# Kernel tuning notes

Measured on AMD Instinct MI355X. Metric: run time of the kernel, lower is better.

Reference implementation:

```python
import jax, jax.numpy as jnp
import numpy as np

N_NODES = 100000
N_EDGES = 3200000
N_FEAT = 512
N_GRAPHS = 64
N_EXTRA_LAYERS = 3  # layers 2..4, all 1->1


def setup_inputs() -> dict:
    key = jax.random.key(0)
    ks = jax.random.split(key, 10)
    x = jax.random.normal(ks[0], (N_NODES, N_FEAT), dtype=jnp.float32)
    edge_src = jax.random.randint(ks[1], (N_EDGES,), 0, N_NODES, dtype=jnp.int32)
    edge_dst = jax.random.randint(ks[2], (N_EDGES,), 0, N_NODES, dtype=jnp.int32)
    graph_ids = jnp.sort(jax.random.randint(ks[3], (N_NODES,), 0, N_GRAPHS, dtype=jnp.int32))
    W_neigh0 = jax.random.normal(ks[4], (N_FEAT, 1), dtype=jnp.float32) * 0.05
    W_self0 = jax.random.normal(ks[5], (N_FEAT, 1), dtype=jnp.float32) * 0.05
    b0 = jax.random.normal(ks[6], (1,), dtype=jnp.float32)
    W_neigh_r = jax.random.normal(ks[7], (N_EXTRA_LAYERS, 1, 1), dtype=jnp.float32)
    W_self_r = jax.random.normal(ks[8], (N_EXTRA_LAYERS, 1, 1), dtype=jnp.float32)
    b_r = jax.random.normal(ks[9], (N_EXTRA_LAYERS, 1), dtype=jnp.float32)
    return {"x": x, "edge_src": edge_src, "edge_dst": edge_dst, "graph_ids": graph_ids,
            "W_neigh0": W_neigh0, "W_self0": W_self0, "b0": b0,
            "W_neigh_r": W_neigh_r, "W_self_r": W_self_r, "b_r": b_r}


def _conv_wl(h, edge_src, edge_dst, W_neigh, W_self, b, n_nodes):
    # GraphConv(norm='none'): project first (in >= out here), gather at src, scatter-sum at dst, + bias
    proj = h @ W_neigh                      # [N, out]
    neigh = jax.ops.segment_sum(proj[edge_src], edge_dst, num_segments=n_nodes) + b
    return neigh + h @ W_self               # residual self-loop linear (no bias)


def reference(x, edge_src, edge_dst, graph_ids, W_neigh0, W_self0, b0, W_neigh_r, W_self_r, b_r):
    n = x.shape[0]
    xs = [x]
    h = jax.nn.relu(_conv_wl(x, edge_src, edge_dst, W_neigh0, W_self0, b0, n))
    xs.append(h)
    for i in range(W_neigh_r.shape[0]):
        h = jax.nn.relu(_conv_wl(h, edge_src, edge_dst, W_neigh_r[i], W_self_r[i], b_r[i], n))
        xs.append(h)
    hcat = jnp.concatenate(xs, axis=1)       # [N, F + num_layers] (concat_features=True)
    # dgl.sum_nodes: per-graph sum over the batched graph
    return jax.ops.segment_sum(hcat, graph_ids, num_segments=N_GRAPHS)  # [G, F + L]
```

## Files before the change

### kernel.cpp

```cpp
#include <hip/hip_runtime.h>

#define N_NODES  100000
#define N_EDGES  3200000
#define N_FEAT   512
#define N_GRAPHS 64
#define N_COLS   516
#define NBINS    1563
#define B1       256
#define EPB      (N_EDGES / B1)
#define CHUNK    25
#define NWAVES   (N_NODES / CHUNK)
#define SRC_MASK 0x1FFFF

__global__ __launch_bounds__(1024) void prep_kernel(
    const int* __restrict__ edst, const int* __restrict__ gid,
    int* __restrict__ histG, int* __restrict__ starts, float* __restrict__ outz)
{
    __shared__ int lh[NBINS];
    const int b = blockIdx.x, tid = threadIdx.x;
    const int gtid = b * 1024 + tid;

    if (gtid < N_GRAPHS * N_COLS) outz[gtid] = 0.f;
    if (gtid < N_NODES) {
        const int g = gid[gtid];
        const int gp = gtid ? gid[gtid - 1] : -1;
        for (int q = gp + 1; q <= g; ++q) starts[q] = gtid;
        if (gtid == N_NODES - 1)
            for (int q = g + 1; q <= N_GRAPHS; ++q) starts[q] = N_NODES;
    }
    for (int i = tid; i < NBINS; i += 1024) lh[i] = 0;
    __syncthreads();
    const int e0 = b * EPB;
    for (int e = e0 + tid; e < e0 + EPB; e += 1024)
        atomicAdd(&lh[edst[e] >> 6], 1);
    __syncthreads();
    for (int i = tid; i < NBINS; i += 1024) histG[i * B1 + b] = lh[i];
}

__device__ __forceinline__ void flush_cs(
    int si, int cur_g, const float a[8], int wave, int lane,
    float* __restrict__ pp, int* __restrict__ pt, float* __restrict__ out)
{
    if (si < 2) {
        const int slot = wave * 2 + si;
        if (lane == 0) pt[slot] = cur_g;
        float* d = pp + (size_t)slot * N_FEAT + lane * 8;
        *(float4*)d       = make_float4(a[0], a[1], a[2], a[3]);
        *(float4*)(d + 4) = make_float4(a[4], a[5], a[6], a[7]);
    } else {
        float* o = out + (size_t)cur_g * N_COLS + lane * 8;
        #pragma unroll
        for (int k = 0; k < 8; ++k) atomicAdd(o + k, a[k]);
    }
}

__global__ __launch_bounds__(256) void pass_x_kernel(
    const float* __restrict__ x, const int* __restrict__ gid,
    const float* __restrict__ wn, const float* __restrict__ ws,
    float* __restrict__ p0, float* __restrict__ s0,
    float* __restrict__ neigh, float* __restrict__ out,
    float* __restrict__ pp, int* __restrict__ pt)
{
    const int wave = (blockIdx.x * blockDim.x + threadIdx.x) >> 6;
    const int lane = threadIdx.x & 63;
    const int start = wave * CHUNK, end = start + CHUNK;

    for (int n = start + lane; n < end; n += 64) neigh[n] = 0.f;

    const float4 wna = *(const float4*)(wn + lane * 8);
    const float4 wnb = *(const float4*)(wn + lane * 8 + 4);
    const float4 wsa = *(const float4*)(ws + lane * 8);
    const float4 wsb = *(const float4*)(ws + lane * 8 + 4);

    float a[8] = {0.f, 0.f, 0.f, 0.f, 0.f, 0.f, 0.f, 0.f};
    int cur_g = gid[start];
    const bool uniform = (gid[end - 1] == cur_g);
    int si = 0;

    for (int n = start; n < end; ++n) {
        if (!uniform) {
            const int g = gid[n];
            if (g != cur_g) {
                flush_cs(si, cur_g, a, wave, lane, pp, pt, out);
                ++si;
                #pragma unroll
                for (int k = 0; k < 8; ++k) a[k] = 0.f;
                cur_g = g;
            }
        }
        const float* row = x + (size_t)n * N_FEAT;
        const float4 xa = *(const float4*)(row + lane * 8);
        const float4 xb = *(const float4*)(row + lane * 8 + 4);

        a[0] += xa.x; a[1] += xa.y; a[2] += xa.z; a[3] += xa.w;
        a[4] += xb.x; a[5] += xb.y; a[6] += xb.z; a[7] += xb.w;

        float dn = xa.x*wna.x + xa.y*wna.y + xa.z*wna.z + xa.w*wna.w
                 + xb.x*wnb.x + xb.y*wnb.y + xb.z*wnb.z + xb.w*wnb.w;
        float dv = xa.x*wsa.x + xa.y*wsa.y + xa.z*wsa.z + xa.w*wsa.w
                 + xb.x*wsb.x + xb.y*wsb.y + xb.z*wsb.z + xb.w*wsb.w;
        #pragma unroll
        for (int off = 32; off > 0; off >>= 1) {
            dn += __shfl_down(dn, off);
            dv += __shfl_down(dv, off);
        }
        if (lane == 0) { p0[n] = dn; s0[n] = dv; }
    }
    flush_cs(si, cur_g, a, wave, lane, pp, pt, out);
    ++si;
    if (lane == 0)
        for (int s2 = si; s2 < 2; ++s2) pt[wave * 2 + s2] = -1;
}

__global__ __launch_bounds__(512) void reduce_x_kernel(
    const float* __restrict__ pp, const int* __restrict__ pt,
    const int* __restrict__ starts, float* __restrict__ out)
{
    const int g = blockIdx.x, c = threadIdx.x;
    const int s = starts[g], e = starts[g + 1];
    float acc = 0.f;
    if (e > s) {
        const int w0 = s / CHUNK, w1 = (e - 1) / CHUNK;
        for (int w = w0; w <= w1; ++w) {
            #pragma unroll
            for (int k = 0; k < 2; ++k) {
                const int slot = w * 2 + k;
                if (pt[slot] == g) acc += pp[(size_t)slot * N_FEAT + c];
            }
        }
    }
    out[(size_t)g * N_COLS + c] += acc;
}

__global__ __launch_bounds__(256) void colscan_kernel(
    const int* __restrict__ histG, int* __restrict__ colscanG,
    int* __restrict__ totalG)
{
    __shared__ int sc[256];
    const int bin = blockIdx.x, t = threadIdx.x;
    const int v = histG[bin * B1 + t];
    sc[t] = v;
    __syncthreads();
    for (int off = 1; off < 256; off <<= 1) {
        const int a = (t >= off) ? sc[t - off] : 0;
        __syncthreads();
        sc[t] += a;
        __syncthreads();
    }
    colscanG[bin * B1 + t] = sc[t] - v;
    if (t == 255) totalG[bin] = sc[255];
}

__global__ __launch_bounds__(256) void scan2_kernel(
    const int* __restrict__ totalG, int* __restrict__ binstart)
{
    __shared__ int sc[256];
    const int t = threadIdx.x;
    const int CH = 7;
    int loc[CH];
    int s = 0;
    for (int i = 0; i < CH; ++i) {
        const int bin = t * CH + i;
        const int v = (bin < NBINS) ? totalG[bin] : 0;
        loc[i] = s; s += v;
    }
    const int my = s;
    sc[t] = my;
    __syncthreads();
    for (int off = 1; off < 256; off <<= 1) {
        const int a = (t >= off) ? sc[t - off] : 0;
        __syncthreads();
        sc[t] += a;
        __syncthreads();
    }
    const int texcl = sc[t] - my;
    for (int i = 0; i < CH; ++i) {
        const int bin = t * CH + i;
        if (bin < NBINS) binstart[bin] = texcl + loc[i];
    }
    if (t == 255) binstart[NBINS] = sc[255];
}

__global__ __launch_bounds__(1024) void reorder_kernel(
    const int* __restrict__ esrc, const int* __restrict__ edst,
    const int* __restrict__ binstart, const int* __restrict__ colscanG,
    int* __restrict__ sorted)
{
    __shared__ int offs[NBINS];
    const int b = blockIdx.x, tid = threadIdx.x;
    for (int i = tid; i < NBINS; i += 1024)
        offs[i] = binstart[i] + colscanG[i * B1 + b];
    __syncthreads();
    const int e0 = b * EPB;
    for (int e = e0 + tid; e < e0 + EPB; e += 1024) {
        const int s = esrc[e], d = edst[e];
        const int p = atomicAdd(&offs[d >> 6], 1);
        sorted[p] = s | ((d & 63) << 17);
    }
}

__global__ __launch_bounds__(256) void binned_scatter_kernel(
    const int* __restrict__ sorted, const int* __restrict__ binstart,
    const float* __restrict__ pin, const float* __restrict__ self_in,
    const float* __restrict__ wself_p, const float* __restrict__ bias_p,
    const float* __restrict__ wnext_p,
    float* __restrict__ h_out, float* __restrict__ p_next,
    const int* __restrict__ gid, float* __restrict__ out, int col)
{
    __shared__ float acc[4][64];
    const int b = blockIdx.x, tid = threadIdx.x;
    ((float*)acc)[tid] = 0.f;
    __syncthreads();

    const int st = binstart[b], en = binstart[b + 1];
    const int w = tid >> 6;
    for (int e = st + tid; e < en; e += 256) {
        const int v = sorted[e];
        atomicAdd(&acc[w][v >> 17], pin[v & SRC_MASK]);
    }
    __syncthreads();

    if (tid < 64) {
        const int n = b * 64 + tid;
        const bool valid = (n < N_NODES);
        float h = 0.f;
        int g = 0;
        if (valid) {
            const float nb = acc[0][tid] + acc[1][tid] + acc[2][tid] + acc[3][tid];
            const float sw = wself_p ? *wself_p : 1.0f;
            const float v = nb + *bias_p + sw * self_in[n];
            h = v > 0.f ? v : 0.f;
            h_out[n] = h;
            if (wnext_p) p_next[n] = h * (*wnext_p);
            g = gid[n];
        }
        const int g0 = __shfl(g, 0);
        if (__all(!valid || g == g0)) {
            float s = h;
            #pragma unroll
            for (int off = 32; off > 0; off >>= 1) s += __shfl_down(s, off);
            if (tid == 0) atomicAdd(&out[(size_t)g0 * N_COLS + col], s);
        } else if (valid) {
            atomicAdd(&out[(size_t)g * N_COLS + col], h);
        }
    }
}

extern "C" void kernel_launch(void* const* d_in, const int* in_sizes, int n_in,
                              void* d_out, int out_size, void* d_ws, size_t ws_size,
                              hipStream_t stream)
{
    (void)in_sizes; (void)n_in; (void)out_size; (void)ws_size;

    const float* x    = (const float*)d_in[0];
    const int*   esrc = (const int*)d_in[1];
    const int*   edst = (const int*)d_in[2];
    const int*   gid  = (const int*)d_in[3];
    const float* Wn0  = (const float*)d_in[4];
    const float* Ws0  = (const float*)d_in[5];
    const float* b0p  = (const float*)d_in[6];
    const float* Wnr  = (const float*)d_in[7];
    const float* Wsr  = (const float*)d_in[8];
    const float* brp  = (const float*)d_in[9];
    float* out = (float*)d_out;

    float* pp    = (float*)d_ws;
    float* bufP  = pp + (size_t)NWAVES * 2 * N_FEAT;
    float* bufP2 = bufP  + N_NODES;
    float* bufS  = bufP2 + N_NODES;
    float* bufH  = bufS  + N_NODES;
    int*   pt       = (int*)(bufH + N_NODES);
    int*   starts   = pt + NWAVES * 2;
    int*   binstart = starts + (N_GRAPHS + 1);
    int*   totalG   = binstart + NBINS + 1;
    int*   histG    = totalG + NBINS;
    int*   colscanG = histG + (size_t)NBINS * B1;
    int*   sorted   = colscanG + (size_t)NBINS * B1;

    prep_kernel<<<B1, 1024, 0, stream>>>(edst, gid, histG, starts, out);
    pass_x_kernel<<<NWAVES / 4, 256, 0, stream>>>(
        x, gid, Wn0, Ws0, bufP, bufS, bufP2 ,
        out, pp, pt);
    colscan_kernel<<<NBINS, 256, 0, stream>>>(histG, colscanG, totalG);
    scan2_kernel<<<1, 256, 0, stream>>>(totalG, binstart);
    reorder_kernel<<<B1, 1024, 0, stream>>>(esrc, edst, binstart, colscanG, sorted);
    reduce_x_kernel<<<N_GRAPHS, 512, 0, stream>>>(pp, pt, starts, out);

    binned_scatter_kernel<<<NBINS, 256, 0, stream>>>(
        sorted, binstart, bufP, bufS, nullptr, b0p, Wnr + 0, bufH, bufP2, gid, out, 512);
    binned_scatter_kernel<<<NBINS, 256, 0, stream>>>(
        sorted, binstart, bufP2, bufH, Wsr + 0, brp + 0, Wnr + 1, bufH, bufP, gid, out, 513);
    binned_scatter_kernel<<<NBINS, 256, 0, stream>>>(
        sorted, binstart, bufP, bufH, Wsr + 1, brp + 1, Wnr + 2, bufH, bufP2, gid, out, 514);
    binned_scatter_kernel<<<NBINS, 256, 0, stream>>>(
        sorted, binstart, bufP2, bufH, Wsr + 2, brp + 2, nullptr, bufH, nullptr, gid, out, 515);
}
```

Baseline: 509.8 us.

## Replace counting-sort edge binning with fixed-capacity buckets fused into feature pass

Drops the histogram, column-scan, global-scan and reorder kernels. Instead, each block writes its edges straight into fixed per-(bin, block) slots of capacity 32, and rare overflows go to a small side list. This bucketing runs in the same launch as the x projection and per-graph column-sum pass. The per-graph reduce of x is folded into the first scatter launch as extra blocks, which cuts the launch count from ten to five. In exchange, each scatter block scans a sparse 8192-slot region plus every block's overflow list. The fixed overflow capacity can silently drop edges if a block overflows more than 64 times.

```diff
diff --git a/kernel.cpp b/kernel.cpp
--- a/kernel.cpp
+++ b/kernel.cpp
@@ -1,4 +1,5 @@
 #include <hip/hip_runtime.h>
+
 
 #define N_NODES  100000
 #define N_EDGES  3200000
@@ -11,228 +12,201 @@
 #define CHUNK    25
 #define NWAVES   (N_NODES / CHUNK)
 #define SRC_MASK 0x1FFFF
-
-__global__ __launch_bounds__(1024) void prep_kernel(
-    const int* __restrict__ edst, const int* __restrict__ gid,
-    int* __restrict__ histG, int* __restrict__ starts, float* __restrict__ outz)
-{
-    __shared__ int lh[NBINS];
-    const int b = blockIdx.x, tid = threadIdx.x;
-    const int gtid = b * 1024 + tid;
-
-    if (gtid < N_GRAPHS * N_COLS) outz[gtid] = 0.f;
-    if (gtid < N_NODES) {
-        const int g = gid[gtid];
-        const int gp = gtid ? gid[gtid - 1] : -1;
-        for (int q = gp + 1; q <= g; ++q) starts[q] = gtid;
-        if (gtid == N_NODES - 1)
-            for (int q = g + 1; q <= N_GRAPHS; ++q) starts[q] = N_NODES;
-    }
-    for (int i = tid; i < NBINS; i += 1024) lh[i] = 0;
-    __syncthreads();
-    const int e0 = b * EPB;
-    for (int e = e0 + tid; e < e0 + EPB; e += 1024)
-        atomicAdd(&lh[edst[e] >> 6], 1);
-    __syncthreads();
-    for (int i = tid; i < NBINS; i += 1024) histG[i * B1 + b] = lh[i];
-}
+#define CAP      32
+#define SLOTS    (B1 * CAP)
+#define OCAP     64
+#define NSLOT    3
 
 __device__ __forceinline__ void flush_cs(
     int si, int cur_g, const float a[8], int wave, int lane,
-    float* __restrict__ pp, int* __restrict__ pt, float* __restrict__ out)
-{
-    if (si < 2) {
-        const int slot = wave * 2 + si;
-        if (lane == 0) pt[slot] = cur_g;
-        float* d = pp + (size_t)slot * N_FEAT + lane * 8;
-        *(float4*)d       = make_float4(a[0], a[1], a[2], a[3]);
-        *(float4*)(d + 4) = make_float4(a[4], a[5], a[6], a[7]);
-    } else {
-        float* o = out + (size_t)cur_g * N_COLS + lane * 8;
-        #pragma unroll
-        for (int k = 0; k < 8; ++k) atomicAdd(o + k, a[k]);
-    }
-}
-
-__global__ __launch_bounds__(256) void pass_x_kernel(
-    const float* __restrict__ x, const int* __restrict__ gid,
+    float* __restrict__ pp, int* __restrict__ pt)
+{
+    const int s = si < NSLOT ? si : NSLOT - 1;
+    const int slot = wave * NSLOT + s;
+    if (lane == 0) pt[slot] = cur_g;
+    float* d = pp + (size_t)slot * N_FEAT + lane * 8;
+    *(float4*)d       = make_float4(a[0], a[1], a[2], a[3]);
+    *(float4*)(d + 4) = make_float4(a[4], a[5], a[6], a[7]);
+}
+
+__global__ __launch_bounds__(256) void fused_k1(
+    const float* __restrict__ x, const int* __restrict__ esrc,
+    const int* __restrict__ edst, const int* __restrict__ gid,
     const float* __restrict__ wn, const float* __restrict__ ws,
     float* __restrict__ p0, float* __restrict__ s0,
-    float* __restrict__ neigh, float* __restrict__ out,
-    float* __restrict__ pp, int* __restrict__ pt)
-{
-    const int wave = (blockIdx.x * blockDim.x + threadIdx.x) >> 6;
-    const int lane = threadIdx.x & 63;
-    const int start = wave * CHUNK, end = start + CHUNK;
-
-    for (int n = start + lane; n < end; n += 64) neigh[n] = 0.f;
-
-    const float4 wna = *(const float4*)(wn + lane * 8);
-    const float4 wnb = *(const float4*)(wn + lane * 8 + 4);
-    const float4 wsa = *(const float4*)(ws + lane * 8);
-    const float4 wsb = *(const float4*)(ws + lane * 8 + 4);
-
-    float a[8] = {0.f, 0.f, 0.f, 0.f, 0.f, 0.f, 0.f, 0.f};
-    int cur_g = gid[start];
-    const bool uniform = (gid[end - 1] == cur_g);
-    int si = 0;
-
-    for (int n = start; n < end; ++n) {
-        if (!uniform) {
-            const int g = gid[n];
-            if (g != cur_g) {
-                flush_cs(si, cur_g, a, wave, lane, pp, pt, out);
-                ++si;
-                #pragma unroll
-                for (int k = 0; k < 8; ++k) a[k] = 0.f;
-                cur_g = g;
-            }
-        }
-        const float* row = x + (size_t)n * N_FEAT;
-        const float4 xa = *(const float4*)(row + lane * 8);
-        const float4 xb = *(const float4*)(row + lane * 8 + 4);
-
-        a[0] += xa.x; a[1] += xa.y; a[2] += xa.z; a[3] += xa.w;
-        a[4] += xb.x; a[5] += xb.y; a[6] += xb.z; a[7] += xb.w;
-
-        float dn = xa.x*wna.x + xa.y*wna.y + xa.z*wna.z + xa.w*wna.w
-                 + xb.x*wnb.x + xb.y*wnb.y + xb.z*wnb.z + xb.w*wnb.w;
-        float dv = xa.x*wsa.x + xa.y*wsa.y + xa.z*wsa.z + xa.w*wsa.w
-                 + xb.x*wsb.x + xb.y*wsb.y + xb.z*wsb.z + xb.w*wsb.w;
-        #pragma unroll
-        for (int off = 32; off > 0; off >>= 1) {
-            dn += __shfl_down(dn, off);
-            dv += __shfl_down(dv, off);
-        }
-        if (lane == 0) { p0[n] = dn; s0[n] = dv; }
-    }
-    flush_cs(si, cur_g, a, wave, lane, pp, pt, out);
-    ++si;
-    if (lane == 0)
-        for (int s2 = si; s2 < 2; ++s2) pt[wave * 2 + s2] = -1;
-}
-
-__global__ __launch_bounds__(512) void reduce_x_kernel(
-    const float* __restrict__ pp, const int* __restrict__ pt,
-    const int* __restrict__ starts, float* __restrict__ out)
-{
-    const int g = blockIdx.x, c = threadIdx.x;
-    const int s = starts[g], e = starts[g + 1];
-    float acc = 0.f;
-    if (e > s) {
-        const int w0 = s / CHUNK, w1 = (e - 1) / CHUNK;
-        for (int w = w0; w <= w1; ++w) {
+    float* __restrict__ out, float* __restrict__ pp, int* __restrict__ pt,
+    int* __restrict__ cntG, int* __restrict__ sorted,
+    int2* __restrict__ ovf, int* __restrict__ ovfcnt,
+    int* __restrict__ starts)
+{
+    __shared__ int cnt[NBINS];
+    __shared__ int ovfc;
+    const int blk = blockIdx.x, tid = threadIdx.x;
+
+    if (blk < 1000) {
+        const int gtid = blk * 256 + tid;
+        if (gtid < N_GRAPHS * N_COLS) out[gtid] = 0.f;
+        if (gtid < N_NODES) {
+            const int g = gid[gtid];
+            const int gp = gtid ? gid[gtid - 1] : -1;
+            for (int q = gp + 1; q <= g; ++q) starts[q] = gtid;
+            if (gtid == N_NODES - 1)
+                for (int q = g + 1; q <= N_GRAPHS; ++q) starts[q] = N_NODES;
+        }
+
+        const int wave = blk * 4 + (tid >> 6);
+        const int lane = tid & 63;
+        const int start = wave * CHUNK, end = start + CHUNK;
+
+        const float4 wna = *(const float4*)(wn + lane * 8);
+        const float4 wnb = *(const float4*)(wn + lane * 8 + 4);
+        const float4 wsa = *(const float4*)(ws + lane * 8);
+        const float4 wsb = *(const float4*)(ws + lane * 8 + 4);
+
+        float a[8] = {0.f, 0.f, 0.f, 0.f, 0.f, 0.f, 0.f, 0.f};
+        int cur_g = gid[start];
+        const bool uniform = (gid[end - 1] == cur_g);
+        int si = 0;
+
+        for (int n = start; n < end; ++n) {
+            if (!uniform) {
+                const int g = gid[n];
+                if (g != cur_g) {
+                    flush_cs(si, cur_g, a, wave, lane, pp, pt);
+                    ++si;
+                    #pragma unroll
+                    for (int k = 0; k < 8; ++k) a[k] = 0.f;
+                    cur_g = g;
+                }
+            }
+            const float* row = x + (size_t)n * N_FEAT;
+            const float4 xa = *(const float4*)(row + lane * 8);
+            const float4 xb = *(const float4*)(row + lane * 8 + 4);
+
+            a[0] += xa.x; a[1] += xa.y; a[2] += xa.z; a[3] += xa.w;
+            a[4] += xb.x; a[5] += xb.y; a[6] += xb.z; a[7] += xb.w;
+
+            float dn = xa.x*wna.x + xa.y*wna.y + xa.z*wna.z + xa.w*wna.w
+                     + xb.x*wnb.x + xb.y*wnb.y + xb.z*wnb.z + xb.w*wnb.w;
+            float dv = xa.x*wsa.x + xa.y*wsa.y + xa.z*wsa.z + xa.w*wsa.w
+                     + xb.x*wsb.x + xb.y*wsb.y + xb.z*wsb.z + xb.w*wsb.w;
             #pragma unroll
-            for (int k = 0; k < 2; ++k) {
-                const int slot = w * 2 + k;
-                if (pt[slot] == g) acc += pp[(size_t)slot * N_FEAT + c];
-            }
-        }
-    }
-    out[(size_t)g * N_COLS + c] += acc;
-}
-
-__global__ __launch_bounds__(256) void colscan_kernel(
-    const int* __restrict__ histG, int* __restrict__ colscanG,
-    int* __restrict__ totalG)
-{
-    __shared__ int sc[256];
-    const int bin = blockIdx.x, t = threadIdx.x;
-    const int v = histG[bin * B1 + t];
-    sc[t] = v;
-    __syncthreads();
-    for (int off = 1; off < 256; off <<= 1) {
-        const int a = (t >= off) ? sc[t - off] : 0;
+            for (int off = 32; off > 0; off >>= 1) {
+                dn += __shfl_down(dn, off);
+                dv += __shfl_down(dv, off);
+            }
+            if (lane == 0) { p0[n] = dn; s0[n] = dv; }
+        }
+        flush_cs(si, cur_g, a, wave, lane, pp, pt);
+        ++si;
+        if (lane == 0)
+            for (int s2 = si; s2 < NSLOT; ++s2) pt[wave * NSLOT + s2] = -1;
+    } else {
+        const int b = blk - 1000;
+        for (int i = tid; i < NBINS; i += 256) cnt[i] = 0;
+        if (tid == 0) ovfc = 0;
         __syncthreads();
-        sc[t] += a;
+
+        const int e0 = b * EPB;
+        for (int e = e0 + tid; e < e0 + EPB; e += 256) {
+            const int s = esrc[e], d = edst[e];
+            const int k = d >> 6;
+            const int r = atomicAdd(&cnt[k], 1);
+            if (r < CAP) {
+                sorted[(size_t)k * SLOTS + b * CAP + r] = s | ((d & 63) << 17);
+            } else {
+                const int q = atomicAdd(&ovfc, 1);
+                if (q < OCAP) ovf[b * OCAP + q] = make_int2(s, d);
+            }
+        }
         __syncthreads();
-    }
-    colscanG[bin * B1 + t] = sc[t] - v;
-    if (t == 255) totalG[bin] = sc[255];
-}
-
-__global__ __launch_bounds__(256) void scan2_kernel(
-    const int* __restrict__ totalG, int* __restrict__ binstart)
-{
-    __shared__ int sc[256];
-    const int t = threadIdx.x;
-    const int CH = 7;
-    int loc[CH];
-    int s = 0;
-    for (int i = 0; i < CH; ++i) {
-        const int bin = t * CH + i;
-        const int v = (bin < NBINS) ? totalG[bin] : 0;
-        loc[i] = s; s += v;
-    }
-    const int my = s;
-    sc[t] = my;
-    __syncthreads();
-    for (int off = 1; off < 256; off <<= 1) {
-        const int a = (t >= off) ? sc[t - off] : 0;
-        __syncthreads();
-        sc[t] += a;
-        __syncthreads();
-    }
-    const int texcl = sc[t] - my;
-    for (int i = 0; i < CH; ++i) {
-        const int bin = t * CH + i;
-        if (bin < NBINS) binstart[bin] = texcl + loc[i];
-    }
-    if (t == 255) binstart[NBINS] = sc[255];
-}
-
-__global__ __launch_bounds__(1024) void reorder_kernel(
-    const int* __restrict__ esrc, const int* __restrict__ edst,
-    const int* __restrict__ binstart, const int* __restrict__ colscanG,
-    int* __restrict__ sorted)
-{
-    __shared__ int offs[NBINS];
-    const int b = blockIdx.x, tid = threadIdx.x;
-    for (int i = tid; i < NBINS; i += 1024)
-        offs[i] = binstart[i] + colscanG[i * B1 + b];
-    __syncthreads();
-    const int e0 = b * EPB;
-    for (int e = e0 + tid; e < e0 + EPB; e += 1024) {
-        const int s = esrc[e], d = edst[e];
-        const int p = atomicAdd(&offs[d >> 6], 1);
-        sorted[p] = s | ((d & 63) << 17);
-    }
-}
-
-__global__ __launch_bounds__(256) void binned_scatter_kernel(
-    const int* __restrict__ sorted, const int* __restrict__ binstart,
+        for (int i = tid; i < NBINS; i += 256) cntG[b * NBINS + i] = cnt[i];
+        if (tid == 0) ovfcnt[b] = ovfc < OCAP ? ovfc : OCAP;
+    }
+}
+
+__global__ __launch_bounds__(256) void scatter_kernel(
+    const int* __restrict__ sorted, const int* __restrict__ cntG,
+    const int2* __restrict__ ovf, const int* __restrict__ ovfcnt,
     const float* __restrict__ pin, const float* __restrict__ self_in,
     const float* __restrict__ wself_p, const float* __restrict__ bias_p,
     const float* __restrict__ wnext_p,
     float* __restrict__ h_out, float* __restrict__ p_next,
-    const int* __restrict__ gid, float* __restrict__ out, int col)
-{
+    const int* __restrict__ gid, float* __restrict__ out, int col,
+    const float* __restrict__ pp, const int* __restrict__ pt,
+    const int* __restrict__ starts, int do_redx)
+{
+    const int k = blockIdx.x, tid = threadIdx.x;
+
+    if (k >= NBINS) {
+        if (!do_redx) return;
+        const int g = k - NBINS;
+        const int s = starts[g], e = starts[g + 1];
+        #pragma unroll
+        for (int cc = 0; cc < 2; ++cc) {
+            const int c = tid + cc * 256;
+            float acc = 0.f;
+            if (e > s) {
+                const int w0 = s / CHUNK, w1 = (e - 1) / CHUNK;
+                for (int w = w0; w <= w1; ++w) {
+                    #pragma unroll
+                    for (int kk = 0; kk < NSLOT; ++kk) {
+                        const int slot = w * NSLOT + kk;
+                        if (pt[slot] == g) acc += pp[(size_t)slot * N_FEAT + c];
+                    }
+                }
+            }
+            out[(size_t)g * N_COLS + c] = acc;
+        }
+        return;
+    }
+
     __shared__ float acc[4][64];
-    const int b = blockIdx.x, tid = threadIdx.x;
+    __shared__ int cntL[B1];
     ((float*)acc)[tid] = 0.f;
+    for (int i = tid; i < B1; i += 256) {
+        const int c = cntG[i * NBINS + k];
+        cntL[i] = c < CAP ? c : CAP;
+    }
+
+    const float sw    = wself_p ? *wself_p : 1.0f;
+    const float bias  = *bias_p;
+    const float wnext = wnext_p ? *wnext_p : 0.0f;
+    const int   n     = k * 64 + tid;
+    const bool  valid = (tid < 64) && (n < N_NODES);
+    float selfv = 0.f;
+    int   g     = 0;
+    if (valid) { selfv = self_in[n]; g = gid[n]; }
     __syncthreads();
 
-    const int st = binstart[b], en = binstart[b + 1];
+    const size_t base = (size_t)k * SLOTS;
     const int w = tid >> 6;
-    for (int e = st + tid; e < en; e += 256) {
-        const int v = sorted[e];
-        atomicAdd(&acc[w][v >> 17], pin[v & SRC_MASK]);
+    for (int slot = tid; slot < SLOTS; slot += 256) {
+        const int bb = slot >> 5;
+        const int i  = slot & (CAP - 1);
+        if (i < cntL[bb]) {
+            const int v = sorted[base + slot];
+            atomicAdd(&acc[w][v >> 17], pin[v & SRC_MASK]);
+        }
+    }
+    for (int b2 = tid; b2 < B1; b2 += 256) {
+        const int oc = ovfcnt[b2];
+        for (int j = 0; j < oc; ++j) {
+            const int2 ee = ovf[b2 * OCAP + j];
+            if ((ee.y >> 6) == k)
+                atomicAdd(&acc[w][ee.y & 63], pin[ee.x]);
+        }
     }
     __syncthreads();
 
     if (tid < 64) {
-        const int n = b * 64 + tid;
-        const bool valid = (n < N_NODES);
         float h = 0.f;
-        int g = 0;
         if (valid) {
             const float nb = acc[0][tid] + acc[1][tid] + acc[2][tid] + acc[3][tid];
-            const float sw = wself_p ? *wself_p : 1.0f;
-            const float v = nb + *bias_p + sw * self_in[n];
+            const float v = nb + bias + sw * selfv;
             h = v > 0.f ? v : 0.f;
             h_out[n] = h;
-            if (wnext_p) p_next[n] = h * (*wnext_p);
-            g = gid[n];
+            if (wnext_p) p_next[n] = h * wnext;
         }
         const int g0 = __shfl(g, 0);
         if (__all(!valid || g == g0)) {
@@ -265,33 +239,31 @@
     float* out = (float*)d_out;
 
     float* pp    = (float*)d_ws;
-    float* bufP  = pp + (size_t)NWAVES * 2 * N_FEAT;
+    float* bufP  = pp + (size_t)NWAVES * NSLOT * N_FEAT;
     float* bufP2 = bufP  + N_NODES;
     float* bufS  = bufP2 + N_NODES;
     float* bufH  = bufS  + N_NODES;
-    int*   pt       = (int*)(bufH + N_NODES);
-    int*   starts   = pt + NWAVES * 2;
-    int*   binstart = starts + (N_GRAPHS + 1);
-    int*   totalG   = binstart + NBINS + 1;
-    int*   histG    = totalG + NBINS;
-    int*   colscanG = histG + (size_t)NBINS * B1;
-    int*   sorted   = colscanG + (size_t)NBINS * B1;
-
-    prep_kernel<<<B1, 1024, 0, stream>>>(edst, gid, histG, starts, out);
-    pass_x_kernel<<<NWAVES / 4, 256, 0, stream>>>(
-        x, gid, Wn0, Ws0, bufP, bufS, bufP2 ,
-        out, pp, pt);
-    colscan_kernel<<<NBINS, 256, 0, stream>>>(histG, colscanG, totalG);
-    scan2_kernel<<<1, 256, 0, stream>>>(totalG, binstart);
-    reorder_kernel<<<B1, 1024, 0, stream>>>(esrc, edst, binstart, colscanG, sorted);
-    reduce_x_kernel<<<N_GRAPHS, 512, 0, stream>>>(pp, pt, starts, out);
-
-    binned_scatter_kernel<<<NBINS, 256, 0, stream>>>(
-        sorted, binstart, bufP, bufS, nullptr, b0p, Wnr + 0, bufH, bufP2, gid, out, 512);
-    binned_scatter_kernel<<<NBINS, 256, 0, stream>>>(
-        sorted, binstart, bufP2, bufH, Wsr + 0, brp + 0, Wnr + 1, bufH, bufP, gid, out, 513);
-    binned_scatter_kernel<<<NBINS, 256, 0, stream>>>(
-        sorted, binstart, bufP, bufH, Wsr + 1, brp + 1, Wnr + 2, bufH, bufP2, gid, out, 514);
-    binned_scatter_kernel<<<NBINS, 256, 0, stream>>>(
-        sorted, binstart, bufP2, bufH, Wsr + 2, brp + 2, nullptr, bufH, nullptr, gid, out, 515);
-}
+    int*   pt     = (int*)(bufH + N_NODES);
+    int*   starts = pt + NWAVES * NSLOT;
+    int*   ovfcnt = starts + 68;
+    int*   cntG   = ovfcnt + 256;
+    int2*  ovf    = (int2*)(cntG + (size_t)B1 * NBINS);
+    int*   sorted = (int*)(ovf + (size_t)B1 * OCAP);
+
+    fused_k1<<<1256, 256, 0, stream>>>(
+        x, esrc, edst, gid, Wn0, Ws0, bufP, bufS, out, pp, pt,
+        cntG, sorted, ovf, ovfcnt, starts);
+
+    scatter_kernel<<<NBINS + N_GRAPHS, 256, 0, stream>>>(
+        sorted, cntG, ovf, ovfcnt, bufP, bufS, nullptr, b0p, Wnr + 0,
+        bufH, bufP2, gid, out, 512, pp, pt, starts, 1);
+    scatter_kernel<<<NBINS + N_GRAPHS, 256, 0, stream>>>(
+        sorted, cntG, ovf, ovfcnt, bufP2, bufH, Wsr + 0, brp + 0, Wnr + 1,
+        bufH, bufP, gid, out, 513, pp, pt, starts, 0);
+    scatter_kernel<<<NBINS + N_GRAPHS, 256, 0, stream>>>(
+        sorted, cntG, ovf, ovfcnt, bufP, bufH, Wsr + 1, brp + 1, Wnr + 2,
+        bufH, bufP2, gid, out, 514, pp, pt, starts, 0);
+    scatter_kernel<<<NBINS + N_GRAPHS, 256, 0, stream>>>(
+        sorted, cntG, ovf, ovfcnt, bufP2, bufH, Wsr + 2, brp + 2, nullptr,
+        bufH, nullptr, gid, out, 515, pp, pt, starts, 0);
+}
```

Measured after the change: 546.5 us. 7.2% more time.
